# Kernel tuning notes

Hardware: AMD Instinct MI355X
Metric: run time of the kernel (lower is better)

The kernel has to match this reference:

```python
import jax, jax.numpy as jnp
import numpy as np

B, DIN, E, H, V = 1024, 512, 512, 1024, 4096
MAX_LEN = 32  # max_len=33 with force_eos=True -> 32 decode steps


def setup_inputs() -> dict:
    key = jax.random.key(0)
    ks = jax.random.split(key, 12)
    def u(k, shape, fan_in):
        s = 1.0 / np.sqrt(fan_in)
        return jax.random.uniform(k, shape, jnp.float32, -s, s)
    return {
        "x": jax.random.normal(ks[0], (B, DIN), jnp.float32),
        "W_agent": u(ks[1], (DIN, H), DIN),
        "b_agent": u(ks[2], (H,), DIN),
        "sos_embedding": 0.01 * jax.random.normal(ks[3], (E,), jnp.float32),
        "emb": jax.random.normal(ks[4], (V, E), jnp.float32),
        "W_ih": u(ks[5], (E, H), H),
        "W_hh": u(ks[6], (H, H), H),
        "b_ih": u(ks[7], (H,), H),
        "b_hh": u(ks[8], (H,), H),
        "W_out": u(ks[9], (H, V), H),
        "b_out": u(ks[10], (V,), H),
    }


def reference(x, W_agent, b_agent, sos_embedding, emb, W_ih, W_hh, b_ih, b_hh, W_out, b_out):
    h0 = x @ W_agent + b_agent                      # agent(x): [B, H]
    inp0 = jnp.broadcast_to(sos_embedding, (x.shape[0], E))

    def step(carry, _):
        inp, h = carry
        h = jnp.tanh(inp @ W_ih + h @ W_hh + b_ih + b_hh)   # RNNCell
        logp = jax.nn.log_softmax(h @ W_out + b_out, axis=1)  # [B, V]
        tok = jnp.argmax(logp, axis=1)                      # eval-mode sample
        lp = jnp.take_along_axis(logp, tok[:, None], axis=1)[:, 0]
        ent = -jnp.sum(jnp.exp(logp) * logp, axis=1)
        return (emb[tok], h), (tok, lp, ent)

    (_, _), (seq, lps, ents) = jax.lax.scan(step, (inp0, h0), None, length=MAX_LEN)
    seq = seq.T        # [B, MAX_LEN]
    lps = lps.T
    ents = ents.T
    # force_eos: append zero column
    zf = jnp.zeros((seq.shape[0], 1), jnp.float32)
    sequence = jnp.concatenate([seq, zf.astype(seq.dtype)], axis=1)
    logits = jnp.concatenate([lps, zf], axis=1)
    entropy = jnp.concatenate([ents, zf], axis=1)
    return sequence, logits, entropy
```

## Files before the change

### kernel.cpp

```cpp
#include <hip/hip_runtime.h>
#include <math.h>

#define B_   1024
#define DIN  512
#define EMB  512
#define H_   1024
#define V_   4096
#define TSTEPS 32
#define LEN  33

typedef __attribute__((ext_vector_type(8))) short short8_t;
typedef __attribute__((ext_vector_type(4))) float f32x4;

#define AH_P  131072
#define AI_P  65536
#define B3_P  196608

__device__ inline unsigned short bf16_rne(float f) {
  unsigned u = __builtin_bit_cast(unsigned, f);
  u += 0x7FFFu + ((u >> 16) & 1u);
  return (unsigned short)(u >> 16);
}
__device__ inline float bf16_to_f(unsigned short h) {
  unsigned u = ((unsigned)h) << 16;
  return __builtin_bit_cast(float, u);
}
struct S3 { short a, b, c; };
__device__ inline S3 split3(float w) {
  unsigned short h0 = bf16_rne(w);  float r1 = w - bf16_to_f(h0);
  unsigned short h1 = bf16_rne(r1); float r2 = r1 - bf16_to_f(h1);
  S3 r; r.a = (short)h0; r.b = (short)h1; r.c = (short)bf16_rne(r2);
  return r;
}

#define T2MERGE(M1,I1,M2,I2, o1,oi1,o2,oi2)                              \
  if (o1 > M1 || (o1 == M1 && oi1 < I1)) {                               \
    float _n2; int _ni2;                                                 \
    if (M1 > o2 || (M1 == o2 && I1 < oi2)) { _n2 = M1; _ni2 = I1; }      \
    else { _n2 = o2; _ni2 = oi2; }                                       \
    M1 = o1; I1 = oi1; M2 = _n2; I2 = _ni2;                              \
  } else if (o1 > M2 || (o1 == M2 && oi1 < I2)) { M2 = o1; I2 = oi1; }

#define GBT 4
#define GKC 256
__global__ __launch_bounds__(256) void k_gemm(
    float* __restrict__ out,
    const float* __restrict__ A1, int K1, const float* __restrict__ W1,
    const float* __restrict__ A2, int K2, const float* __restrict__ W2,
    const float* __restrict__ b1, const float* __restrict__ b2,
    int do_tanh)
{
  const int N = H_;
  __shared__ float sA[GBT][GKC];
  const int tid = threadIdx.x;
  const int bid = blockIdx.x;
  const int colb = (bid & 7) >> 1;
  const int rowb = ((bid >> 3) << 1) | (bid & 1);
  const int rb  = rowb * GBT;
  const int col = colb * 256 + tid;

  float acc[GBT];
  float bias = b1[col] + (b2 ? b2[col] : 0.0f);
#pragma unroll
  for (int r = 0; r < GBT; ++r) acc[r] = bias;

  const int nch = (K1 + K2) / GKC;
  for (int c = 0; c < nch; ++c) {
    const int kb = c * GKC;
    const float* A; const float* W; int k0, strideA;
    if (kb < K1) { A = A1; W = W1; k0 = kb;      strideA = K1; }
    else         { A = A2; W = W2; k0 = kb - K1; strideA = K2; }
    __syncthreads();
    {
      int r = tid >> 6, kk = (tid & 63) << 2;
      *(float4*)&sA[r][kk] = *(const float4*)(A + (size_t)(rb + r) * strideA + k0 + kk);
    }
    __syncthreads();
    const float* Wp = W + (size_t)k0 * N + col;
#pragma unroll 4
    for (int k = 0; k < GKC; k += 4) {
      float4 a0 = *(const float4*)&sA[0][k];
      float4 a1 = *(const float4*)&sA[1][k];
      float4 a2 = *(const float4*)&sA[2][k];
      float4 a3 = *(const float4*)&sA[3][k];
      float w0 = Wp[(size_t)k * N];
      float w1 = Wp[(size_t)(k + 1) * N];
      float w2 = Wp[(size_t)(k + 2) * N];
      float w3 = Wp[(size_t)(k + 3) * N];
      acc[0] = fmaf(a0.x, w0, acc[0]); acc[1] = fmaf(a1.x, w0, acc[1]);
      acc[2] = fmaf(a2.x, w0, acc[2]); acc[3] = fmaf(a3.x, w0, acc[3]);
      acc[0] = fmaf(a0.y, w1, acc[0]); acc[1] = fmaf(a1.y, w1, acc[1]);
      acc[2] = fmaf(a2.y, w1, acc[2]); acc[3] = fmaf(a3.y, w1, acc[3]);
      acc[0] = fmaf(a0.z, w2, acc[0]); acc[1] = fmaf(a1.z, w2, acc[1]);
      acc[2] = fmaf(a2.z, w2, acc[2]); acc[3] = fmaf(a3.z, w2, acc[3]);
      acc[0] = fmaf(a0.w, w3, acc[0]); acc[1] = fmaf(a1.w, w3, acc[1]);
      acc[2] = fmaf(a2.w, w3, acc[2]); acc[3] = fmaf(a3.w, w3, acc[3]);
    }
  }
#pragma unroll
  for (int r = 0; r < GBT; ++r) {
    float v = acc[r];
    if (do_tanh) v = tanhf(v);
    out[(size_t)(rb + r) * N + col] = v;
  }
}

__global__ __launch_bounds__(256) void k_prepack(
    const float* __restrict__ W, unsigned short* __restrict__ Bp)
{
  int t = blockIdx.x * 256 + threadIdx.x;
  int lane = t & 63;
  int ntg  = (t >> 6) & 255;
  int ks   = t >> 14;
  int col  = ntg * 16 + (lane & 15);
  int krow = ks * 32 + ((lane >> 4) << 3);
  short8_t hv;
#pragma unroll
  for (int j = 0; j < 8; ++j) {
    float w = W[(size_t)(krow + j) * V_ + col];
    hv[j] = (short)bf16_rne(w);
  }
  size_t base = ((size_t)ks * 256 + ntg) * 64 + lane;
  ((short8_t*)Bp)[base] = hv;
}

__global__ __launch_bounds__(256) void k_packW3(
    const float* __restrict__ Wih, const float* __restrict__ Whh,
    unsigned short* __restrict__ BU)
{
  int t = blockIdx.x * 256 + threadIdx.x;
  int lane = t & 63;
  int ntg  = (t >> 6) & 63;
  int ks   = t >> 12;
  int col  = ntg * 16 + (lane & 15);
  int krow = ks * 32 + ((lane >> 4) << 3);
  short8_t p0, p1, p2;
#pragma unroll
  for (int j = 0; j < 8; ++j) {
    int kr = krow + j;
    float w = (kr < DIN) ? Wih[(size_t)kr * H_ + col]
                         : Whh[(size_t)(kr - DIN) * H_ + col];
    S3 s = split3(w);
    p0[j] = s.a; p1[j] = s.b; p2[j] = s.c;
  }
  short8_t* o = (short8_t*)BU;
  size_t base = ((size_t)ks * 64 + ntg) * 64 + lane;
  o[base] = p0; o[base + B3_P] = p1; o[base + 2 * B3_P] = p2;
}

__global__ __launch_bounds__(256) void k_wtrans(
    const float* __restrict__ W, float* __restrict__ WT)
{
  __shared__ float tile[64][65];
  int kb = (blockIdx.x & 15) * 64;
  int vb = (blockIdx.x >> 4) * 64;
  int t = threadIdx.x;
  {
    int vv = t & 63, k0 = (t >> 6) * 16;
    for (int j = 0; j < 16; ++j)
      tile[k0 + j][vv] = W[(size_t)(kb + k0 + j) * V_ + vb + vv];
  }
  __syncthreads();
  {
    int kk = t & 63, v0 = (t >> 6) * 16;
    for (int j = 0; j < 16; ++j)
      WT[(size_t)(vb + v0 + j) * H_ + kb + kk] = tile[kk][v0 + j];
  }
}

__global__ __launch_bounds__(256) void k_packh(
    const float* __restrict__ h, unsigned short* __restrict__ AU)
{
  int t = blockIdx.x * 256 + threadIdx.x;
  int r = t >> 7, q = t & 127;
  int ks = q >> 2, kg = q & 3;
  int lanep = (r & 15) + (kg << 4);
  int rt = r >> 4;
  const float* src = h + (size_t)r * H_ + q * 8;
  float4 f0 = *(const float4*)src;
  float4 f1 = *(const float4*)(src + 4);
  float f[8] = {f0.x, f0.y, f0.z, f0.w, f1.x, f1.y, f1.z, f1.w};
  short8_t p0, p1, p2;
#pragma unroll
  for (int j = 0; j < 8; ++j) {
    S3 s = split3(f[j]);
    p0[j] = s.a; p1[j] = s.b; p2[j] = s.c;
  }
  short8_t* o = (short8_t*)AU;
  size_t base = (size_t)rt * 2048 + (size_t)ks * 64 + lanep;
  o[base] = p0; o[base + AH_P] = p1; o[base + 2 * AH_P] = p2;
}

__global__ __launch_bounds__(256) void k_sos3(
    const float* __restrict__ sos, unsigned short* __restrict__ AU)
{
  int wid = threadIdx.x >> 6, lane = threadIdx.x & 63;
  int row = blockIdx.x * 4 + wid;
  const float* src = sos + lane * 8;
  float4 f0 = *(const float4*)src;
  float4 f1 = *(const float4*)(src + 4);
  float f[8] = {f0.x, f0.y, f0.z, f0.w, f1.x, f1.y, f1.z, f1.w};
  short8_t p0, p1, p2;
#pragma unroll
  for (int j = 0; j < 8; ++j) {
    S3 s = split3(f[j]);
    p0[j] = s.a; p1[j] = s.b; p2[j] = s.c;
  }
  int ks = lane >> 2, kg = lane & 3;
  int lanep = (row & 15) + (kg << 4);
  int rt = row >> 4;
  short8_t* o = (short8_t*)AU;
  size_t base = (size_t)rt * 1024 + (size_t)ks * 64 + lanep;
  o[base] = p0; o[base + AI_P] = p1; o[base + 2 * AI_P] = p2;
}

__global__ __launch_bounds__(512) void k_rnn(
    const unsigned short* __restrict__ AinpU, const unsigned short* __restrict__ AhU,
    const unsigned short* __restrict__ Bw3U,
    const float* __restrict__ b1, const float* __restrict__ b2,
    float* __restrict__ hout, unsigned short* __restrict__ AhOutU)
{
  __shared__ float sh[64][65];
  const short8_t* Ainp = (const short8_t*)AinpU;
  const short8_t* Ah   = (const short8_t*)AhU;
  const short8_t* Bw3  = (const short8_t*)Bw3U;

  const int bid  = blockIdx.x;
  const int colb = ((bid & 7) << 1) | ((bid >> 3) & 1);
  const int rowb = bid >> 4;
  const int tid  = threadIdx.x, lane = tid & 63, wid = tid >> 6;
  const int wm = (wid >> 1) & 1, wn = wid & 1, kh = wid >> 2;
  const int l15 = lane & 15, lg = lane >> 4;

  f32x4 acc[2][2];
#pragma unroll
  for (int rt = 0; rt < 2; ++rt)
#pragma unroll
    for (int nt = 0; nt < 2; ++nt) {
      int col = colb * 64 + wn * 32 + nt * 16 + l15;
      float b = (kh == 0) ? (b1[col] + b2[col]) : 0.0f;
      acc[rt][nt] = (f32x4){b, b, b, b};
    }

  const int rt0 = rowb * 4 + wm * 2;
  const int ng0 = colb * 4 + wn * 2;
  const int ks0 = kh * 24;

#define RNN_LOAD(A_, B_, KS)                                                   \
  {                                                                            \
    int _ks = (KS);                                                            \
    if (_ks < 16) {                                                            \
      _Pragma("unroll") for (int rt = 0; rt < 2; ++rt)                         \
        _Pragma("unroll") for (int p = 0; p < 3; ++p)                          \
          A_[rt][p] = Ainp[(size_t)p * AI_P + (size_t)(rt0 + rt) * 1024 +      \
                           (size_t)_ks * 64 + lane];                           \
    } else {                                                                   \
      int _h = _ks - 16;                                                       \
      _Pragma("unroll") for (int rt = 0; rt < 2; ++rt)                         \
        _Pragma("unroll") for (int p = 0; p < 3; ++p)                          \
          A_[rt][p] = Ah[(size_t)p * AH_P + (size_t)(rt0 + rt) * 2048 +        \
                         (size_t)_h * 64 + lane];                              \
    }                                                                          \
    _Pragma("unroll") for (int nt = 0; nt < 2; ++nt)                           \
      _Pragma("unroll") for (int p = 0; p < 3; ++p)                            \
        B_[nt][p] = Bw3[(size_t)p * B3_P + (size_t)_ks * 4096 +                \
                        (size_t)(ng0 + nt) * 64 + lane];                       \
  }

  short8_t a[2][3], bb[2][3];
  RNN_LOAD(a, bb, ks0)
#pragma unroll
  for (int i = 0; i < 24; ++i) {
    short8_t an[2][3], bn[2][3];
    if (i < 23) RNN_LOAD(an, bn, ks0 + i + 1)
#pragma unroll
    for (int rt = 0; rt < 2; ++rt)
#pragma unroll
      for (int nt = 0; nt < 2; ++nt) {
        acc[rt][nt] = __builtin_amdgcn_mfma_f32_16x16x32_bf16(a[rt][0], bb[nt][0], acc[rt][nt], 0, 0, 0);
        acc[rt][nt] = __builtin_amdgcn_mfma_f32_16x16x32_bf16(a[rt][0], bb[nt][1], acc[rt][nt], 0, 0, 0);
        acc[rt][nt] = __builtin_amdgcn_mfma_f32_16x16x32_bf16(a[rt][1], bb[nt][0], acc[rt][nt], 0, 0, 0);
        acc[rt][nt] = __builtin_amdgcn_mfma_f32_16x16x32_bf16(a[rt][1], bb[nt][1], acc[rt][nt], 0, 0, 0);
        acc[rt][nt] = __builtin_amdgcn_mfma_f32_16x16x32_bf16(a[rt][0], bb[nt][2], acc[rt][nt], 0, 0, 0);
        acc[rt][nt] = __builtin_amdgcn_mfma_f32_16x16x32_bf16(a[rt][2], bb[nt][0], acc[rt][nt], 0, 0, 0);
      }
    if (i < 23) {
#pragma unroll
      for (int rt = 0; rt < 2; ++rt)
#pragma unroll
        for (int p = 0; p < 3; ++p) { a[rt][p] = an[rt][p]; bb[rt][p] = bn[rt][p]; }
    }
  }
#undef RNN_LOAD

  if (kh == 1) {
#pragma unroll
    for (int rt = 0; rt < 2; ++rt)
#pragma unroll
      for (int nt = 0; nt < 2; ++nt)
#pragma unroll
        for (int r = 0; r < 4; ++r)
          sh[wm * 32 + rt * 16 + lg * 4 + r][wn * 32 + nt * 16 + l15] = acc[rt][nt][r];
  }
  __syncthreads();
  if (kh == 0) {
#pragma unroll
    for (int rt = 0; rt < 2; ++rt)
#pragma unroll
      for (int nt = 0; nt < 2; ++nt)
#pragma unroll
        for (int r = 0; r < 4; ++r) {
          int lr = wm * 32 + rt * 16 + lg * 4 + r;
          int lc = wn * 32 + nt * 16 + l15;
          float v = tanhf(acc[rt][nt][r] + sh[lr][lc]);
          hout[(size_t)(rowb * 64 + lr) * H_ + colb * 64 + lc] = v;
          sh[lr][lc] = v;
        }
  }
  __syncthreads();
  {
    int lr = tid >> 3, q = tid & 7;
    int gk = colb * 64 + q * 8;
    int ks = gk >> 5, kg = (gk >> 3) & 3;
    int gr = rowb * 64 + lr;
    int lanep = (gr & 15) + (kg << 4);
    int rt = gr >> 4;
    short8_t p0, p1, p2;
#pragma unroll
    for (int j = 0; j < 8; ++j) {
      S3 s = split3(sh[lr][q * 8 + j]);
      p0[j] = s.a; p1[j] = s.b; p2[j] = s.c;
    }
    short8_t* o = (short8_t*)AhOutU;
    size_t base = (size_t)rt * 2048 + (size_t)ks * 64 + lanep;
    o[base] = p0; o[base + AH_P] = p1; o[base + 2 * AH_P] = p2;
  }
}

__global__ __launch_bounds__(512) void k_logits3(
    const unsigned short* __restrict__ AhU, const unsigned short* __restrict__ BpU,
    const float* __restrict__ bout, float4* __restrict__ partA,
    float4* __restrict__ partB)
{
  __shared__ float sh[64][128];
  __shared__ float sred[2][2][32][6];
  __shared__ float sbmax[64];
  const short8_t* Ah = (const short8_t*)AhU;
  const short8_t* Bp = (const short8_t*)BpU;

  const int bid  = blockIdx.x;
  const int colb = ((bid & 7) << 2) | ((bid >> 3) & 3);
  const int rowb = bid >> 5;
  const int tid  = threadIdx.x, lane = tid & 63, wid = tid >> 6;
  const int wm = (wid >> 1) & 1, wn = wid & 1, kh = wid >> 2;
  const int l15 = lane & 15, lg = lane >> 4;

  const int colbase = colb * 128 + wn * 64;
  f32x4 acc[2][4];
#pragma unroll
  for (int nt = 0; nt < 4; ++nt) {
    float b = (kh == 0) ? bout[colbase + nt * 16 + l15] : 0.0f;
    acc[0][nt] = (f32x4){b, b, b, b};
    acc[1][nt] = acc[0][nt];
  }
  const int rt0 = rowb * 4 + wm * 2;
  const int ng0 = colb * 8 + wn * 4;
  const int ks0 = kh * 16;

#define LG_LOAD(A_, B_, KS)                                                    \
  {                                                                            \
    int _ks = (KS);                                                            \
    _Pragma("unroll") for (int rt = 0; rt < 2; ++rt)                           \
      A_[rt] = Ah[(size_t)(rt0 + rt) * 2048 + (size_t)_ks * 64 + lane];        \
    _Pragma("unroll") for (int nt = 0; nt < 4; ++nt)                           \
      B_[nt] = Bp[((size_t)_ks * 256 + ng0 + nt) * 64 + lane];                 \
  }

  short8_t abuf[3][2], bbuf[3][4];
  LG_LOAD(abuf[0], bbuf[0], ks0)
  LG_LOAD(abuf[1], bbuf[1], ks0 + 1)
#pragma unroll
  for (int i = 0; i < 16; ++i) {
    const int cur = i % 3, nxt = (i + 2) % 3;
    if (i + 2 < 16) LG_LOAD(abuf[nxt], bbuf[nxt], ks0 + i + 2)
#pragma unroll
    for (int rt = 0; rt < 2; ++rt)
#pragma unroll
      for (int nt = 0; nt < 4; ++nt)
        acc[rt][nt] = __builtin_amdgcn_mfma_f32_16x16x32_bf16(
            abuf[cur][rt], bbuf[cur][nt], acc[rt][nt], 0, 0, 0);
  }
#undef LG_LOAD

  if (kh == 1) {
#pragma unroll
    for (int rt = 0; rt < 2; ++rt)
#pragma unroll
      for (int nt = 0; nt < 4; ++nt)
#pragma unroll
        for (int r = 0; r < 4; ++r)
          sh[wm * 32 + rt * 16 + lg * 4 + r][wn * 64 + nt * 16 + l15] = acc[rt][nt][r];
  }
  __syncthreads();
  if (kh == 0) {
#pragma unroll
    for (int rt = 0; rt < 2; ++rt)
#pragma unroll
      for (int nt = 0; nt < 4; ++nt)
#pragma unroll
        for (int r = 0; r < 4; ++r)
          acc[rt][nt][r] += sh[wm * 32 + rt * 16 + lg * 4 + r][wn * 64 + nt * 16 + l15];
  }

  if (kh == 0) {
#pragma unroll
    for (int rt = 0; rt < 2; ++rt)
#pragma unroll
      for (int r = 0; r < 4; ++r) {
        float M1 = -1e30f, M2 = -1e30f; int I1 = 0, I2 = 0;
#pragma unroll
        for (int nt = 0; nt < 4; ++nt) {
          float v = acc[rt][nt][r]; int c = colbase + nt * 16 + l15;
          if (v > M1) { M2 = M1; I2 = I1; M1 = v; I1 = c; }
          else if (v > M2) { M2 = v; I2 = c; }
        }
#pragma unroll
        for (int d = 1; d < 16; d <<= 1) {
          float o1 = __shfl_xor(M1, d); int oi1 = __shfl_xor(I1, d);
          float o2 = __shfl_xor(M2, d); int oi2 = __shfl_xor(I2, d);
          T2MERGE(M1, I1, M2, I2, o1, oi1, o2, oi2)
        }
        if (l15 == 0) {
          int rl = rt * 16 + lg * 4 + r;
          sred[wm][wn][rl][0] = M1; sred[wm][wn][rl][1] = (float)I1;
          sred[wm][wn][rl][2] = M2; sred[wm][wn][rl][3] = (float)I2;
        }
      }
  }
  __syncthreads();
  if (tid < 64) {
    int wmm = tid >> 5, rl = tid & 31;
    float M1 = sred[wmm][0][rl][0]; int I1 = (int)sred[wmm][0][rl][1];
    float M2 = sred[wmm][0][rl][2]; int I2 = (int)sred[wmm][0][rl][3];
    float o1 = sred[wmm][1][rl][0]; int oi1 = (int)sred[wmm][1][rl][1];
    float o2 = sred[wmm][1][rl][2]; int oi2 = (int)sred[wmm][1][rl][3];
    T2MERGE(M1, I1, M2, I2, o1, oi1, o2, oi2)
    int row = rowb * 64 + wmm * 32 + rl;
    partA[(size_t)row * 32 + colb] = make_float4(M1, (float)I1, M2, (float)I2);
    sbmax[wmm * 32 + rl] = M1;
  }
  __syncthreads();
  if (kh == 0) {
#pragma unroll
    for (int rt = 0; rt < 2; ++rt)
#pragma unroll
      for (int r = 0; r < 4; ++r) {
        float m = sbmax[wm * 32 + rt * 16 + lg * 4 + r];
        float s = 0.f, tsum = 0.f;
#pragma unroll
        for (int nt = 0; nt < 4; ++nt) {
          float d = acc[rt][nt][r] - m;
          float e = expf(d);
          s += e; tsum += d * e;
        }
#pragma unroll
        for (int d = 1; d < 16; d <<= 1) { s += __shfl_xor(s, d); tsum += __shfl_xor(tsum, d); }
        if (l15 == 0) {
          int rl = rt * 16 + lg * 4 + r;
          sred[wm][wn][rl][4] = s; sred[wm][wn][rl][5] = tsum;
        }
      }
  }
  __syncthreads();
  if (tid < 64) {
    int wmm = tid >> 5, rl = tid & 31;
    float s = sred[wmm][0][rl][4] + sred[wmm][1][rl][4];
    float tsum = sred[wmm][0][rl][5] + sred[wmm][1][rl][5];
    int row = rowb * 64 + wmm * 32 + rl;
    partB[(size_t)row * 32 + colb] = make_float4(s, tsum, 0.f, 0.f);
  }
}

__global__ __launch_bounds__(256) void k_finalize3(
    const float4* __restrict__ partA, const float4* __restrict__ partB,
    const float* __restrict__ h, const float* __restrict__ Wout,
    const float* __restrict__ WoutT, const float* __restrict__ bout,
    const float* __restrict__ emb, float* __restrict__ out,
    unsigned short* __restrict__ AinpU, int tstep)
{
  const int lane = threadIdx.x & 63;
  const int wid  = threadIdx.x >> 6;
  const int row  = blockIdx.x * 4 + wid;

  float M1 = -1e30f, M2 = -1e30f; int I1 = 0, I2 = 0;
  float bm = -1e30f, s_l = 0.f, t_l = 0.f;
  if (lane < 32) {
    float4 pa = partA[(size_t)row * 32 + lane];
    float4 pb = partB[(size_t)row * 32 + lane];
    M1 = pa.x; I1 = (int)pa.y; M2 = pa.z; I2 = (int)pa.w;
    bm = pa.x; s_l = pb.x; t_l = pb.y;
  }
  for (int d = 1; d < 32; d <<= 1) {
    float o1 = __shfl_xor(M1, d); int oi1 = __shfl_xor(I1, d);
    float o2 = __shfl_xor(M2, d); int oi2 = __shfl_xor(I2, d);
    T2MERGE(M1, I1, M2, I2, o1, oi1, o2, oi2)
  }
  M1 = __shfl(M1, 0); I1 = __shfl(I1, 0);
  M2 = __shfl(M2, 0); I2 = __shfl(I2, 0);

  float e = (lane < 32) ? expf(bm - M1) : 0.f;
  float s = e * s_l;
  float tsum = e * (t_l + (bm - M1) * s_l);
  for (int d = 1; d < 64; d <<= 1) { s += __shfl_xor(s, d); tsum += __shfl_xor(tsum, d); }

  const float* hrow = h + (size_t)row * H_;
  float d1 = 0.f, d2 = 0.f;
  if (WoutT) {
    const float* w1 = WoutT + (size_t)I1 * H_;
    const float* w2 = WoutT + (size_t)I2 * H_;
#pragma unroll 4
    for (int k = lane; k < H_; k += 64) {
      float hv = hrow[k];
      d1 = fmaf(hv, w1[k], d1);
      d2 = fmaf(hv, w2[k], d2);
    }
  } else {
    for (int k = lane; k < H_; k += 64) {
      float hv = hrow[k];
      d1 = fmaf(hv, Wout[(size_t)k * V_ + I1], d1);
      d2 = fmaf(hv, Wout[(size_t)k * V_ + I2], d2);
    }
  }
  for (int d = 1; d < 64; d <<= 1) { d1 += __shfl_xor(d1, d); d2 += __shfl_xor(d2, d); }
  d1 += bout[I1]; d2 += bout[I2];

  int tok; float ltok;
  if (d2 > d1 || (d2 == d1 && I2 < I1)) { tok = I2; ltok = d2; }
  else                                  { tok = I1; ltok = d1; }
  float lg_s = logf(s);
  if (lane == 0) {
    out[(size_t)row * LEN + tstep]                  = (float)tok;
    out[(size_t)(B_ * LEN) + row * LEN + tstep]     = ltok - M1 - lg_s;
    out[(size_t)(2 * B_ * LEN) + row * LEN + tstep] = lg_s - tsum / s;
  }
  const float* er = emb + (size_t)tok * EMB + lane * 8;
  float4 f0 = *(const float4*)er;
  float4 f1 = *(const float4*)(er + 4);
  float f[8] = {f0.x, f0.y, f0.z, f0.w, f1.x, f1.y, f1.z, f1.w};
  short8_t p0, p1, p2;
#pragma unroll
  for (int j = 0; j < 8; ++j) {
    S3 s3v = split3(f[j]);
    p0[j] = s3v.a; p1[j] = s3v.b; p2[j] = s3v.c;
  }
  int ks = lane >> 2, kg = lane & 3;
  int lanep = (row & 15) + (kg << 4);
  int rt = row >> 4;
  short8_t* o = (short8_t*)AinpU;
  size_t base = (size_t)rt * 1024 + (size_t)ks * 64 + lanep;
  o[base] = p0; o[base + AI_P] = p1; o[base + 2 * AI_P] = p2;
}

#define BT 16
#define KC 128
__global__ __launch_bounds__(256) void k_logits_f32(
    const float* __restrict__ h, const float* __restrict__ Wout,
    const float* __restrict__ bout, float4* __restrict__ part)
{
  __shared__ float sA[BT][KC];
  __shared__ float redf[4][BT];
  __shared__ float redf2[4][BT];
  __shared__ int   redi[4][BT];
  __shared__ float bm[BT];

  const int tid = threadIdx.x;
  const int rb  = blockIdx.x * BT;
  const int c0  = blockIdx.y * 512 + tid * 2;

  float acc[BT][2];
  float2 bj = *(const float2*)(bout + c0);
#pragma unroll
  for (int r = 0; r < BT; ++r) { acc[r][0] = bj.x; acc[r][1] = bj.y; }

  for (int kb = 0; kb < H_; kb += KC) {
    __syncthreads();
    {
      float4* s4 = (float4*)sA;
#pragma unroll
      for (int i = 0; i < 2; ++i) {
        int idx = tid + i * 256;
        int r = idx >> 5, kk = (idx & 31) << 2;
        s4[idx] = *(const float4*)(h + (size_t)(rb + r) * H_ + kb + kk);
      }
    }
    __syncthreads();
    const float* Wp = Wout + (size_t)kb * V_ + c0;
#pragma unroll 2
    for (int k = 0; k < KC; k += 4) {
      float4 a[BT];
#pragma unroll
      for (int r = 0; r < BT; ++r) a[r] = *((const float4*)sA[r] + (k >> 2));
      float2 w[4];
#pragma unroll
      for (int u = 0; u < 4; ++u) w[u] = *(const float2*)(Wp + (size_t)(k + u) * V_);
#pragma unroll
      for (int u = 0; u < 4; ++u)
#pragma unroll
        for (int r = 0; r < BT; ++r) {
          float av = ((const float*)&a[r])[u];
          acc[r][0] = fmaf(av, w[u].x, acc[r][0]);
          acc[r][1] = fmaf(av, w[u].y, acc[r][1]);
        }
    }
  }

  const int wid = tid >> 6, lane = tid & 63;
  float mx[BT]; int ix[BT];
#pragma unroll
  for (int r = 0; r < BT; ++r) {
    float m = acc[r][0]; int ii = c0;
    if (acc[r][1] > m) { m = acc[r][1]; ii = c0 + 1; }
    mx[r] = m; ix[r] = ii;
  }
#pragma unroll
  for (int r = 0; r < BT; ++r) {
    for (int d = 32; d; d >>= 1) {
      float ov = __shfl_xor(mx[r], d);
      int   oi = __shfl_xor(ix[r], d);
      if (ov > mx[r] || (ov == mx[r] && oi < ix[r])) { mx[r] = ov; ix[r] = oi; }
    }
  }
  if (lane == 0) {
#pragma unroll
    for (int r = 0; r < BT; ++r) { redf[wid][r] = mx[r]; redi[wid][r] = ix[r]; }
  }
  __syncthreads();
  if (tid < BT) {
    float m = redf[0][tid]; int ii = redi[0][tid];
    for (int w = 1; w < 4; ++w) {
      float ov = redf[w][tid]; int oi = redi[w][tid];
      if (ov > m || (ov == m && oi < ii)) { m = ov; ii = oi; }
    }
    bm[tid] = m; redi[0][tid] = ii;
  }
  __syncthreads();
  float ss[BT], tt[BT];
#pragma unroll
  for (int r = 0; r < BT; ++r) {
    float m = bm[r];
    float s = 0.f, t = 0.f;
#pragma unroll
    for (int j = 0; j < 2; ++j) {
      float d = acc[r][j] - m;
      float e2 = expf(d);
      s += e2; t += d * e2;
    }
    ss[r] = s; tt[r] = t;
  }
#pragma unroll
  for (int r = 0; r < BT; ++r) {
    for (int d = 32; d; d >>= 1) {
      ss[r] += __shfl_xor(ss[r], d);
      tt[r] += __shfl_xor(tt[r], d);
    }
  }
  if (lane == 0) {
#pragma unroll
    for (int r = 0; r < BT; ++r) { redf[wid][r] = ss[r]; redf2[wid][r] = tt[r]; }
  }
  __syncthreads();
  if (tid < BT) {
    float s = 0.f, t = 0.f;
    for (int w = 0; w < 4; ++w) { s += redf[w][tid]; t += redf2[w][tid]; }
    part[(size_t)(rb + tid) * 8 + blockIdx.y] =
        make_float4(bm[tid], s, t, (float)redi[0][tid]);
  }
}

__global__ __launch_bounds__(128) void k_finalize_f32(
    const float4* __restrict__ part, const float* __restrict__ emb,
    float* __restrict__ out, float* __restrict__ inp, int t)
{
  const int row = blockIdx.x;
  __shared__ int s_tok;
  if (threadIdx.x == 0) {
    float4 p[8];
#pragma unroll
    for (int i = 0; i < 8; ++i) p[i] = part[(size_t)row * 8 + i];
    float m = p[0].x; int tok = (int)p[0].w;
#pragma unroll
    for (int i = 1; i < 8; ++i)
      if (p[i].x > m) { m = p[i].x; tok = (int)p[i].w; }
    float S = 0.f, T = 0.f;
#pragma unroll
    for (int i = 0; i < 8; ++i) {
      float w = expf(p[i].x - m);
      S += w * p[i].y;
      T += w * (p[i].z + (p[i].x - m) * p[i].y);
    }
    float lp  = -logf(S);
    float ent = logf(S) - T / S;
    out[(size_t)row * LEN + t]                  = (float)tok;
    out[(size_t)(B_ * LEN) + row * LEN + t]     = lp;
    out[(size_t)(2 * B_ * LEN) + row * LEN + t] = ent;
    s_tok = tok;
  }
  __syncthreads();
  const float4* src = (const float4*)(emb + (size_t)s_tok * EMB);
  float4* dst = (float4*)(inp + (size_t)row * EMB);
  for (int i = threadIdx.x; i < EMB / 4; i += blockDim.x) dst[i] = src[i];
}

__global__ void k_sos(const float* __restrict__ sos, float* __restrict__ inp) {
  int i = blockIdx.x * blockDim.x + threadIdx.x;
  ((float4*)inp)[i] = ((const float4*)sos)[i & (EMB / 4 - 1)];
}
__global__ void k_zero(float* __restrict__ out) {
  int i = blockIdx.x * blockDim.x + threadIdx.x;
  if (i < 3 * B_) {
    int sec = i >> 10, row = i & (B_ - 1);
    out[(size_t)sec * (B_ * LEN) + (size_t)row * LEN + (LEN - 1)] = 0.f;
  }
}

extern "C" void kernel_launch(void* const* d_in, const int* in_sizes, int n_in,
                              void* d_out, int out_size, void* d_ws, size_t ws_size,
                              hipStream_t stream) {
  const float* x       = (const float*)d_in[0];
  const float* W_agent = (const float*)d_in[1];
  const float* b_agent = (const float*)d_in[2];
  const float* sos     = (const float*)d_in[3];
  const float* emb     = (const float*)d_in[4];
  const float* W_ih    = (const float*)d_in[5];
  const float* W_hh    = (const float*)d_in[6];
  const float* b_ih    = (const float*)d_in[7];
  const float* b_hh    = (const float*)d_in[8];
  const float* W_out   = (const float*)d_in[9];
  const float* b_out   = (const float*)d_in[10];
  float* out = (float*)d_out;

  const size_t SZ_BPOUT = 8388608;
  const size_t SZ_BW3   = 9437184;
  const size_t SZ_WT    = 16777216;
  const size_t SZ_AH    = 6291456;
  const size_t SZ_AINP  = 3145728;
  const size_t SZ_H     = 4194304;
  const size_t SZ_PART  = 524288;
  const size_t NEED_A = SZ_BPOUT + SZ_BW3 + SZ_WT + 2 * SZ_AH + SZ_AINP + SZ_H + 2 * SZ_PART;
  const size_t NEED_B = NEED_A - SZ_WT;

  if (ws_size >= NEED_B) {
    const bool useT = ws_size >= NEED_A;
    char* p = (char*)d_ws;
    unsigned short* BpOut = (unsigned short*)p; p += SZ_BPOUT;
    unsigned short* Bw3   = (unsigned short*)p; p += SZ_BW3;
    float* WoutT = nullptr;
    if (useT) { WoutT = (float*)p; p += SZ_WT; }
    unsigned short* Ah0  = (unsigned short*)p; p += SZ_AH;
    unsigned short* Ah1  = (unsigned short*)p; p += SZ_AH;
    unsigned short* Ainp = (unsigned short*)p; p += SZ_AINP;
    float*  hbuf  = (float*)p; p += SZ_H;
    float4* partA = (float4*)p; p += SZ_PART;
    float4* partB = (float4*)p;

    k_sos3<<<dim3(256), dim3(256), 0, stream>>>(sos, Ainp);
    k_prepack<<<dim3(2048), dim3(256), 0, stream>>>(W_out, BpOut);
    k_packW3<<<dim3(768), dim3(256), 0, stream>>>(W_ih, W_hh, Bw3);
    if (useT) k_wtrans<<<dim3(1024), dim3(256), 0, stream>>>(W_out, WoutT);
    k_gemm<<<dim3(1024), dim3(256), 0, stream>>>(
        hbuf, x, DIN, W_agent, nullptr, 0, nullptr, b_agent, nullptr, 0);
    k_packh<<<dim3(512), dim3(256), 0, stream>>>(hbuf, Ah0);

    for (int t = 0; t < TSTEPS; ++t) {
      unsigned short* AhIn  = (t & 1) ? Ah1 : Ah0;
      unsigned short* AhOut = (t & 1) ? Ah0 : Ah1;
      k_rnn<<<dim3(256), dim3(512), 0, stream>>>(
          Ainp, AhIn, Bw3, b_ih, b_hh, hbuf, AhOut);
      k_logits3<<<dim3(512), dim3(512), 0, stream>>>(
          AhOut, BpOut, b_out, partA, partB);
      k_finalize3<<<dim3(256), dim3(256), 0, stream>>>(
          partA, partB, hbuf, W_out, WoutT, b_out, emb, out, Ainp, t);
    }
  } else {
    float*  h0buf = (float*)d_ws;
    float*  h1buf = h0buf + (size_t)B_ * H_;
    float*  inp   = h1buf + (size_t)B_ * H_;
    float4* part  = (float4*)(inp + (size_t)B_ * EMB);

    k_sos<<<dim3(B_ * EMB / 4 / 256), dim3(256), 0, stream>>>(sos, inp);
    k_gemm<<<dim3(1024), dim3(256), 0, stream>>>(
        h0buf, x, DIN, W_agent, nullptr, 0, nullptr, b_agent, nullptr, 0);
    for (int t = 0; t < TSTEPS; ++t) {
      float* hr = (t & 1) ? h1buf : h0buf;
      float* hw = (t & 1) ? h0buf : h1buf;
      k_gemm<<<dim3(1024), dim3(256), 0, stream>>>(
          hw, inp, EMB, W_ih, hr, H_, W_hh, b_ih, b_hh, 1);
      k_logits_f32<<<dim3(B_ / BT, V_ / 512), dim3(256), 0, stream>>>(
          hw, W_out, b_out, part);
      k_finalize_f32<<<dim3(B_), dim3(128), 0, stream>>>(part, emb, out, inp, t);
    }
  }
  k_zero<<<dim3(12), dim3(256), 0, stream>>>(out);
}
```

Measured before the change: 1.969 ms.

## Widen logits kernel tile to 64x256 with 4x4 MFMA tiles per wave

The logits GEMM block tile grows from 64x128 to 64x256, so each wave now computes a 64x64 sub-tile (4x4 MFMA tiles) instead of 32x64, and the grid drops from 512 to 256 blocks. Partial softmax/argmax results now come in 16 column blocks instead of 32, and the finalize kernel is adjusted to reduce 16 partials. The goal is more data reuse per loaded A/B fragment and less partial-reduction traffic. In exchange it uses more registers per wave, adds LDS padding, and leaves fewer blocks to fill the GPU, which may reduce occupancy and latency hiding.

```diff
diff --git a/kernel.cpp b/kernel.cpp
--- a/kernel.cpp
+++ b/kernel.cpp
@@ -337,84 +337,95 @@
   }
 }
 
-__global__ __launch_bounds__(512) void k_logits3(
+__global__ __launch_bounds__(512) void k_logits4(
     const unsigned short* __restrict__ AhU, const unsigned short* __restrict__ BpU,
     const float* __restrict__ bout, float4* __restrict__ partA,
     float4* __restrict__ partB)
 {
-  __shared__ float sh[64][128];
-  __shared__ float sred[2][2][32][6];
+  __shared__ float sh[64][260];
+  __shared__ float sred[4][64][6];
   __shared__ float sbmax[64];
   const short8_t* Ah = (const short8_t*)AhU;
   const short8_t* Bp = (const short8_t*)BpU;
 
   const int bid  = blockIdx.x;
-  const int colb = ((bid & 7) << 2) | ((bid >> 3) & 3);
-  const int rowb = bid >> 5;
+  const int colb = ((bid & 7) << 1) | ((bid >> 3) & 1);
+  const int rowb = bid >> 4;
   const int tid  = threadIdx.x, lane = tid & 63, wid = tid >> 6;
-  const int wm = (wid >> 1) & 1, wn = wid & 1, kh = wid >> 2;
+  const int wn = wid & 3, kh = wid >> 2;
   const int l15 = lane & 15, lg = lane >> 4;
 
-  const int colbase = colb * 128 + wn * 64;
-  f32x4 acc[2][4];
+  const int colbase = colb * 256 + wn * 64;
+  f32x4 acc[4][4];
 #pragma unroll
   for (int nt = 0; nt < 4; ++nt) {
     float b = (kh == 0) ? bout[colbase + nt * 16 + l15] : 0.0f;
     acc[0][nt] = (f32x4){b, b, b, b};
-    acc[1][nt] = acc[0][nt];
-  }
-  const int rt0 = rowb * 4 + wm * 2;
-  const int ng0 = colb * 8 + wn * 4;
+    acc[1][nt] = acc[0][nt]; acc[2][nt] = acc[0][nt]; acc[3][nt] = acc[0][nt];
+  }
+  const int rt0 = rowb * 4;
+  const int ng0 = colb * 16 + wn * 4;
   const int ks0 = kh * 16;
 
-#define LG_LOAD(A_, B_, KS)                                                    \
+#define LG4_LOAD(A_, B_, KS)                                                   \
   {                                                                            \
-    int _ks = (KS);                                                            \
-    _Pragma("unroll") for (int rt = 0; rt < 2; ++rt)                           \
+    const int _ks = (KS);                                                      \
+    _Pragma("unroll") for (int rt = 0; rt < 4; ++rt)                           \
       A_[rt] = Ah[(size_t)(rt0 + rt) * 2048 + (size_t)_ks * 64 + lane];        \
     _Pragma("unroll") for (int nt = 0; nt < 4; ++nt)                           \
       B_[nt] = Bp[((size_t)_ks * 256 + ng0 + nt) * 64 + lane];                 \
   }
-
-  short8_t abuf[3][2], bbuf[3][4];
-  LG_LOAD(abuf[0], bbuf[0], ks0)
-  LG_LOAD(abuf[1], bbuf[1], ks0 + 1)
-#pragma unroll
-  for (int i = 0; i < 16; ++i) {
-    const int cur = i % 3, nxt = (i + 2) % 3;
-    if (i + 2 < 16) LG_LOAD(abuf[nxt], bbuf[nxt], ks0 + i + 2)
-#pragma unroll
-    for (int rt = 0; rt < 2; ++rt)
+#define LG4_MFMA(A_, B_)                                                       \
+  _Pragma("unroll") for (int rt = 0; rt < 4; ++rt)                             \
+    _Pragma("unroll") for (int nt = 0; nt < 4; ++nt)                           \
+      acc[rt][nt] = __builtin_amdgcn_mfma_f32_16x16x32_bf16(                   \
+          A_[rt], B_[nt], acc[rt][nt], 0, 0, 0);
+
+  short8_t a0[4], b0[4], a1[4], b1[4];
+  LG4_LOAD(a0, b0, ks0 + 0)
+  LG4_LOAD(a1, b1, ks0 + 1)
+  LG4_MFMA(a0, b0) LG4_LOAD(a0, b0, ks0 + 2)
+  LG4_MFMA(a1, b1) LG4_LOAD(a1, b1, ks0 + 3)
+  LG4_MFMA(a0, b0) LG4_LOAD(a0, b0, ks0 + 4)
+  LG4_MFMA(a1, b1) LG4_LOAD(a1, b1, ks0 + 5)
+  LG4_MFMA(a0, b0) LG4_LOAD(a0, b0, ks0 + 6)
+  LG4_MFMA(a1, b1) LG4_LOAD(a1, b1, ks0 + 7)
+  LG4_MFMA(a0, b0) LG4_LOAD(a0, b0, ks0 + 8)
+  LG4_MFMA(a1, b1) LG4_LOAD(a1, b1, ks0 + 9)
+  LG4_MFMA(a0, b0) LG4_LOAD(a0, b0, ks0 + 10)
+  LG4_MFMA(a1, b1) LG4_LOAD(a1, b1, ks0 + 11)
+  LG4_MFMA(a0, b0) LG4_LOAD(a0, b0, ks0 + 12)
+  LG4_MFMA(a1, b1) LG4_LOAD(a1, b1, ks0 + 13)
+  LG4_MFMA(a0, b0) LG4_LOAD(a0, b0, ks0 + 14)
+  LG4_MFMA(a1, b1) LG4_LOAD(a1, b1, ks0 + 15)
+  LG4_MFMA(a0, b0)
+  LG4_MFMA(a1, b1)
+#undef LG4_LOAD
+#undef LG4_MFMA
+
+  if (kh == 1) {
+#pragma unroll
+    for (int rt = 0; rt < 4; ++rt)
 #pragma unroll
       for (int nt = 0; nt < 4; ++nt)
-        acc[rt][nt] = __builtin_amdgcn_mfma_f32_16x16x32_bf16(
-            abuf[cur][rt], bbuf[cur][nt], acc[rt][nt], 0, 0, 0);
-  }
-#undef LG_LOAD
-
-  if (kh == 1) {
-#pragma unroll
-    for (int rt = 0; rt < 2; ++rt)
+#pragma unroll
+        for (int r = 0; r < 4; ++r)
+          sh[rt * 16 + lg * 4 + r][wn * 64 + nt * 16 + l15] = acc[rt][nt][r];
+  }
+  __syncthreads();
+  if (kh == 0) {
+#pragma unroll
+    for (int rt = 0; rt < 4; ++rt)
 #pragma unroll
       for (int nt = 0; nt < 4; ++nt)
 #pragma unroll
         for (int r = 0; r < 4; ++r)
-          sh[wm * 32 + rt * 16 + lg * 4 + r][wn * 64 + nt * 16 + l15] = acc[rt][nt][r];
-  }
-  __syncthreads();
+          acc[rt][nt][r] += sh[rt * 16 + lg * 4 + r][wn * 64 + nt * 16 + l15];
+  }
+
   if (kh == 0) {
 #pragma unroll
-    for (int rt = 0; rt < 2; ++rt)
-#pragma unroll
-      for (int nt = 0; nt < 4; ++nt)
-#pragma unroll
-        for (int r = 0; r < 4; ++r)
-          acc[rt][nt][r] += sh[wm * 32 + rt * 16 + lg * 4 + r][wn * 64 + nt * 16 + l15];
-  }
-
-  if (kh == 0) {
-#pragma unroll
-    for (int rt = 0; rt < 2; ++rt)
+    for (int rt = 0; rt < 4; ++rt)
 #pragma unroll
       for (int r = 0; r < 4; ++r) {
         float M1 = -1e30f, M2 = -1e30f; int I1 = 0, I2 = 0;
@@ -432,30 +443,33 @@
         }
         if (l15 == 0) {
           int rl = rt * 16 + lg * 4 + r;
-          sred[wm][wn][rl][0] = M1; sred[wm][wn][rl][1] = (float)I1;
-          sred[wm][wn][rl][2] = M2; sred[wm][wn][rl][3] = (float)I2;
+          sred[wn][rl][0] = M1; sred[wn][rl][1] = (float)I1;
+          sred[wn][rl][2] = M2; sred[wn][rl][3] = (float)I2;
         }
       }
   }
   __syncthreads();
   if (tid < 64) {
-    int wmm = tid >> 5, rl = tid & 31;
-    float M1 = sred[wmm][0][rl][0]; int I1 = (int)sred[wmm][0][rl][1];
-    float M2 = sred[wmm][0][rl][2]; int I2 = (int)sred[wmm][0][rl][3];
-    float o1 = sred[wmm][1][rl][0]; int oi1 = (int)sred[wmm][1][rl][1];
-    float o2 = sred[wmm][1][rl][2]; int oi2 = (int)sred[wmm][1][rl][3];
-    T2MERGE(M1, I1, M2, I2, o1, oi1, o2, oi2)
-    int row = rowb * 64 + wmm * 32 + rl;
-    partA[(size_t)row * 32 + colb] = make_float4(M1, (float)I1, M2, (float)I2);
-    sbmax[wmm * 32 + rl] = M1;
+    int rl = tid;
+    float M1 = sred[0][rl][0]; int I1 = (int)sred[0][rl][1];
+    float M2 = sred[0][rl][2]; int I2 = (int)sred[0][rl][3];
+#pragma unroll
+    for (int w = 1; w < 4; ++w) {
+      float o1 = sred[w][rl][0]; int oi1 = (int)sred[w][rl][1];
+      float o2 = sred[w][rl][2]; int oi2 = (int)sred[w][rl][3];
+      T2MERGE(M1, I1, M2, I2, o1, oi1, o2, oi2)
+    }
+    int row = rowb * 64 + rl;
+    partA[(size_t)row * 16 + colb] = make_float4(M1, (float)I1, M2, (float)I2);
+    sbmax[rl] = M1;
   }
   __syncthreads();
   if (kh == 0) {
 #pragma unroll
-    for (int rt = 0; rt < 2; ++rt)
+    for (int rt = 0; rt < 4; ++rt)
 #pragma unroll
       for (int r = 0; r < 4; ++r) {
-        float m = sbmax[wm * 32 + rt * 16 + lg * 4 + r];
+        float m = sbmax[rt * 16 + lg * 4 + r];
         float s = 0.f, tsum = 0.f;
 #pragma unroll
         for (int nt = 0; nt < 4; ++nt) {
@@ -467,17 +481,17 @@
         for (int d = 1; d < 16; d <<= 1) { s += __shfl_xor(s, d); tsum += __shfl_xor(tsum, d); }
         if (l15 == 0) {
           int rl = rt * 16 + lg * 4 + r;
-          sred[wm][wn][rl][4] = s; sred[wm][wn][rl][5] = tsum;
+          sred[wn][rl][4] = s; sred[wn][rl][5] = tsum;
         }
       }
   }
   __syncthreads();
   if (tid < 64) {
-    int wmm = tid >> 5, rl = tid & 31;
-    float s = sred[wmm][0][rl][4] + sred[wmm][1][rl][4];
-    float tsum = sred[wmm][0][rl][5] + sred[wmm][1][rl][5];
-    int row = rowb * 64 + wmm * 32 + rl;
-    partB[(size_t)row * 32 + colb] = make_float4(s, tsum, 0.f, 0.f);
+    int rl = tid;
+    float s = sred[0][rl][4] + sred[1][rl][4] + sred[2][rl][4] + sred[3][rl][4];
+    float tsum = sred[0][rl][5] + sred[1][rl][5] + sred[2][rl][5] + sred[3][rl][5];
+    int row = rowb * 64 + rl;
+    partB[(size_t)row * 16 + colb] = make_float4(s, tsum, 0.f, 0.f);
   }
 }
 
@@ -494,13 +508,13 @@
 
   float M1 = -1e30f, M2 = -1e30f; int I1 = 0, I2 = 0;
   float bm = -1e30f, s_l = 0.f, t_l = 0.f;
-  if (lane < 32) {
-    float4 pa = partA[(size_t)row * 32 + lane];
-    float4 pb = partB[(size_t)row * 32 + lane];
+  if (lane < 16) {
+    float4 pa = partA[(size_t)row * 16 + lane];
+    float4 pb = partB[(size_t)row * 16 + lane];
     M1 = pa.x; I1 = (int)pa.y; M2 = pa.z; I2 = (int)pa.w;
     bm = pa.x; s_l = pb.x; t_l = pb.y;
   }
-  for (int d = 1; d < 32; d <<= 1) {
+  for (int d = 1; d < 16; d <<= 1) {
     float o1 = __shfl_xor(M1, d); int oi1 = __shfl_xor(I1, d);
     float o2 = __shfl_xor(M2, d); int oi2 = __shfl_xor(I2, d);
     T2MERGE(M1, I1, M2, I2, o1, oi1, o2, oi2)
@@ -508,7 +522,7 @@
   M1 = __shfl(M1, 0); I1 = __shfl(I1, 0);
   M2 = __shfl(M2, 0); I2 = __shfl(I2, 0);
 
-  float e = (lane < 32) ? expf(bm - M1) : 0.f;
+  float e = (lane < 16) ? expf(bm - M1) : 0.f;
   float s = e * s_l;
   float tsum = e * (t_l + (bm - M1) * s_l);
   for (int d = 1; d < 64; d <<= 1) { s += __shfl_xor(s, d); tsum += __shfl_xor(tsum, d); }
@@ -776,7 +790,7 @@
       unsigned short* AhOut = (t & 1) ? Ah0 : Ah1;
       k_rnn<<<dim3(256), dim3(512), 0, stream>>>(
           Ainp, AhIn, Bw3, b_ih, b_hh, hbuf, AhOut);
-      k_logits3<<<dim3(512), dim3(512), 0, stream>>>(
+      k_logits4<<<dim3(256), dim3(512), 0, stream>>>(
           AhOut, BpOut, b_out, partA, partB);
       k_finalize3<<<dim3(256), dim3(256), 0, stream>>>(
           partA, partB, hbuf, W_out, WoutT, b_out, emb, out, Ainp, t);
```

Result: slower. 2.395 ms (+21.6%).
